# Kernel tuning notes

Measured on AMD Instinct MI355X. Metric: run time of the kernel, lower is better.

## Reference

```python
import jax, jax.numpy as jnp
import numpy as np

N, NFEAT = 8192, 128

def _unif(k, shape, fan_out):
    s = 1.0 / np.sqrt(fan_out)
    return jax.random.uniform(k, shape, jnp.float32, -s, s)

def setup_inputs() -> dict:
    key = jax.random.key(0)
    ks = jax.random.split(key, 10)
    x = jax.random.normal(ks[0], (N, NFEAT), jnp.float32)
    adj = jax.random.uniform(ks[1], (N, N), jnp.float32)  # all > 0 -> full degree
    W1 = _unif(ks[2], (NFEAT, 10), 10); b1 = _unif(ks[3], (10,), 10)
    W2 = _unif(ks[4], (10, 5), 5);      b2 = _unif(ks[5], (5,), 5)
    fc1_W = _unif(ks[6], (5, 5), 5);    fc1_b = _unif(ks[7], (5,), 5)
    fc_W = _unif(ks[8], (5, 2), 2);     fc_b = _unif(ks[9], (2,), 2)
    return dict(x=x, adj=adj, W1=W1, b1=b1, W2=W2, b2=b2,
                fc1_W=fc1_W, fc1_b=fc1_b, fc_W=fc_W, fc_b=fc_b)

def _gcn(x, adj, W, b):
    # D = diag(row-wise count of adj > 0); A_tilda = D^-1/2 (A + I) D^-1/2
    deg = jnp.sum((adj > 0.0).astype(x.dtype), axis=1)
    dinv = deg ** -0.5                       # [N]
    s = (x @ W) * dinv[:, None]              # D^-1/2 @ (X W), [N, out]
    out = dinv[:, None] * (adj @ s + s)      # D^-1/2 @ (A + I) @ s
    return out + b

def reference(x, adj, W1, b1, W2, b2, fc1_W, fc1_b, fc_W, fc_b):
    h = jax.nn.relu(_gcn(x, adj, W1, b1))    # [N, 10]
    h = _gcn(h, adj, W2, b2)                 # [N, 5]
    z = jax.nn.relu(jnp.mean(h, axis=0))     # [5]
    z2 = jax.nn.relu(z @ fc1_W + fc1_b)      # [5]
    y = jax.nn.sigmoid(z2 @ fc_W + fc_b)     # [2]
    return (z, y)
```

## Files before the change

kernel.cpp:

```cpp
#include <hip/hip_runtime.h>
#include <math.h>

#define NN 8192
#define NF 128


__device__ __forceinline__ float comp4(const float4& v, int c) {
    return c == 0 ? v.x : c == 1 ? v.y : c == 2 ? v.z : v.w;
}

__global__ __launch_bounds__(256) void kS1p(const float* __restrict__ x,
                                            const float* __restrict__ W1,
                                            float* __restrict__ s1p) {
    __shared__ float sW[NF * 10];
    for (int i = threadIdx.x; i < NF * 10; i += 256) sW[i] = W1[i];
    __syncthreads();
    int tid = blockIdx.x * 256 + threadIdx.x;
    int j = tid / 10, k = tid % 10;
    const float4* xr = (const float4*)(x + (size_t)j * NF);
    float s = 0.f;
#pragma unroll
    for (int f4 = 0; f4 < 32; f4++) {
        float4 a = xr[f4];
        s += a.x * sW[(f4 * 4 + 0) * 10 + k] + a.y * sW[(f4 * 4 + 1) * 10 + k]
           + a.z * sW[(f4 * 4 + 2) * 10 + k] + a.w * sW[(f4 * 4 + 3) * 10 + k];
    }
    s1p[tid] = s;
}

__global__ __launch_bounds__(512) void kFuse(const float* __restrict__ adj,
                                             const float* __restrict__ s1p,
                                             float* __restrict__ accO,
                                             float* __restrict__ dinv,
                                             float* __restrict__ c0,
                                             int* __restrict__ Zcount,
                                             int* __restrict__ Zlist) {
    __shared__ float lcs[4][2048];
    const int t = threadIdx.x;
    const int lane = t & 63, wid = t >> 6;
    for (int n = t; n < 8192; n += 512) ((float*)lcs)[n] = 0.f;
    __syncthreads();

    const int i0 = blockIdx.x * 32 + wid * 4;
    float acc[4][10];
#pragma unroll
    for (int r = 0; r < 4; r++)
#pragma unroll
        for (int k = 0; k < 10; k++) acc[r][k] = 0.f;
    float rmin[4] = {1e30f, 1e30f, 1e30f, 1e30f};

    const float4* a0p = (const float4*)(adj + (size_t)(i0 + 0) * NN);
    const float4* a1p = (const float4*)(adj + (size_t)(i0 + 1) * NN);
    const float4* a2p = (const float4*)(adj + (size_t)(i0 + 2) * NN);
    const float4* a3p = (const float4*)(adj + (size_t)(i0 + 3) * NN);
    const float4* spB = (const float4*)s1p;

    auto loadT = [&](float4 (&A)[4], float4 (&S)[10], int v) {
        A[0] = a0p[v]; A[1] = a1p[v]; A[2] = a2p[v]; A[3] = a3p[v];
#pragma unroll
        for (int q = 0; q < 10; q++) S[q] = spB[(size_t)v * 10 + q];
    };

    auto computeT = [&](const float4 (&A)[4], const float4 (&S)[10], int v) {
        atomicAdd(&lcs[0][v], A[0].x + A[1].x + A[2].x + A[3].x);
        atomicAdd(&lcs[1][v], A[0].y + A[1].y + A[2].y + A[3].y);
        atomicAdd(&lcs[2][v], A[0].z + A[1].z + A[2].z + A[3].z);
        atomicAdd(&lcs[3][v], A[0].w + A[1].w + A[2].w + A[3].w);
#pragma unroll
        for (int r = 0; r < 4; r++)
            rmin[r] = fminf(rmin[r], fminf(fminf(A[r].x, A[r].y), fminf(A[r].z, A[r].w)));
#pragma unroll
        for (int jj = 0; jj < 4; jj++) {
            const float a0c = comp4(A[0], jj), a1c = comp4(A[1], jj);
            const float a2c = comp4(A[2], jj), a3c = comp4(A[3], jj);
#pragma unroll
            for (int k = 0; k < 10; k++) {
                const int idx = jj * 10 + k;
                const float s = comp4(S[idx >> 2], idx & 3);
                acc[0][k] = fmaf(a0c, s, acc[0][k]);
                acc[1][k] = fmaf(a1c, s, acc[1][k]);
                acc[2][k] = fmaf(a2c, s, acc[2][k]);
                acc[3][k] = fmaf(a3c, s, acc[3][k]);
            }
        }
    };

    float4 Aa[4], Ba[4];
    float4 As[10], Bs[10];
    int vi = lane;
    loadT(Aa, As, vi);
#pragma unroll 1
    for (int it = 0; it < 15; it++) {
        loadT(Ba, Bs, vi + 64);
        computeT(Aa, As, vi);
        loadT(Aa, As, vi + 128);
        computeT(Ba, Bs, vi + 64);
        vi += 128;
    }
    loadT(Ba, Bs, vi + 64);
    computeT(Aa, As, vi);
    computeT(Ba, Bs, vi + 64);

#pragma unroll
    for (int r = 0; r < 4; r++)
#pragma unroll
        for (int k = 0; k < 10; k++)
#pragma unroll
            for (int off = 32; off > 0; off >>= 1)
                acc[r][k] += __shfl_xor(acc[r][k], off, 64);

    const float dinv0 = rsqrtf((float)NN);
#pragma unroll
    for (int r = 0; r < 4; r++) {
        unsigned long long anyz = __ballot(rmin[r] <= 0.f);
        if (lane == 0) {
            const int i = i0 + r;
            dinv[i] = dinv0;
            if (anyz) { int p = atomicAdd(Zcount, 1); Zlist[p] = i; }
#pragma unroll
            for (int k = 0; k < 10; k++) accO[i * 10 + k] = acc[r][k];
        }
    }

    __syncthreads();
    for (int n = t; n < 8192; n += 512)
        atomicAdd(&c0[n], lcs[n & 3][n >> 2]);
}

__global__ __launch_bounds__(256) void kZdeg(const float* __restrict__ adj,
                                             const int* __restrict__ Zcount,
                                             const int* __restrict__ Zlist,
                                             float* __restrict__ dinv) {
    __shared__ int wsum[4];
    const int lane = threadIdx.x & 63, wid = threadIdx.x >> 6;
    const int zc = *Zcount;
    for (int p = blockIdx.x; p < zc; p += gridDim.x) {
        const int zi = Zlist[p];
        const float4* ar = (const float4*)(adj + (size_t)zi * NN);
        int cnt = 0;
        for (int v = threadIdx.x; v < 2048; v += 256) {
            float4 a = ar[v];
            cnt += (a.x > 0.f) + (a.y > 0.f) + (a.z > 0.f) + (a.w > 0.f);
        }
#pragma unroll
        for (int off = 32; off > 0; off >>= 1) cnt += __shfl_xor(cnt, off, 64);
        if (lane == 0) wsum[wid] = cnt;
        __syncthreads();
        if (threadIdx.x == 0)
            dinv[zi] = rsqrtf((float)(wsum[0] + wsum[1] + wsum[2] + wsum[3]));
        __syncthreads();
    }
}

__global__ __launch_bounds__(256) void kTail(const float* __restrict__ adj,
                                             const float* __restrict__ accI,
                                             const float* __restrict__ s1p,
                                             const float* __restrict__ dinv,
                                             const float* __restrict__ c0,
                                             const int* __restrict__ Zcount,
                                             const int* __restrict__ Zlist,
                                             const float* __restrict__ b1,
                                             const float* __restrict__ W2,
                                             float* __restrict__ accum) {
    const int j = blockIdx.x * 256 + threadIdx.x;
    const float dinv0 = rsqrtf((float)NN);
    const float dj = dinv[j];
    float cj = c0[j] * dinv0;
    float hv[10];
#pragma unroll
    for (int k = 0; k < 10; k++) hv[k] = dinv0 * accI[j * 10 + k];

    const int zc = *Zcount;
    for (int p = 0; p < zc; p++) {
        const int zi = Zlist[p];
        const float dz = dinv[zi] - dinv0;
        cj += dz * adj[(size_t)zi * NN + j];
        const float az = dz * adj[(size_t)j * NN + zi];
#pragma unroll
        for (int k = 0; k < 10; k++) hv[k] += az * s1p[zi * 10 + k];
    }
#pragma unroll
    for (int k = 0; k < 10; k++)
        hv[k] = fmaxf(dj * (hv[k] + dj * s1p[j * 10 + k]) + b1[k], 0.f);

    float p10[10];
#pragma unroll
    for (int k = 0; k < 5; k++) {
        float s = 0.f;
#pragma unroll
        for (int m = 0; m < 10; m++) s += hv[m] * W2[m * 5 + k];
        s *= dj;
        p10[k] = cj * s;
        p10[5 + k] = dj * s;
    }
#pragma unroll
    for (int q = 0; q < 10; q++) {
        float v = p10[q];
#pragma unroll
        for (int off = 32; off > 0; off >>= 1) v += __shfl_xor(v, off, 64);
        if ((threadIdx.x & 63) == 0) atomicAdd(&accum[q], v);
    }
}

__global__ void kF2(const float* __restrict__ accum, const float* __restrict__ b2,
                    const float* __restrict__ fc1W, const float* __restrict__ fc1b,
                    const float* __restrict__ fcW, const float* __restrict__ fcb,
                    float* __restrict__ out) {
    if (threadIdx.x == 0 && blockIdx.x == 0) {
        float z[5];
        for (int k = 0; k < 5; k++) {
            float v = (accum[k] + accum[5 + k]) * (1.f / (float)NN) + b2[k];
            z[k] = fmaxf(v, 0.f);
            out[k] = z[k];
        }
        float z2[5];
        for (int m = 0; m < 5; m++) {
            float v = fc1b[m];
            for (int k = 0; k < 5; k++) v += z[k] * fc1W[k * 5 + m];
            z2[m] = fmaxf(v, 0.f);
        }
        for (int n = 0; n < 2; n++) {
            float v = fcb[n];
            for (int m = 0; m < 5; m++) v += z2[m] * fcW[m * 2 + n];
            out[5 + n] = 1.f / (1.f + expf(-v));
        }
    }
}

extern "C" void kernel_launch(void* const* d_in, const int* in_sizes, int n_in,
                              void* d_out, int out_size, void* d_ws, size_t ws_size,
                              hipStream_t stream) {
    const float* x    = (const float*)d_in[0];
    const float* adj  = (const float*)d_in[1];
    const float* W1   = (const float*)d_in[2];
    const float* b1   = (const float*)d_in[3];
    const float* W2   = (const float*)d_in[4];
    const float* b2   = (const float*)d_in[5];
    const float* fc1W = (const float*)d_in[6];
    const float* fc1b = (const float*)d_in[7];
    const float* fcW  = (const float*)d_in[8];
    const float* fcb  = (const float*)d_in[9];
    (void)in_sizes; (void)n_in; (void)out_size; (void)ws_size;

    float* ws    = (float*)d_ws;
    float* dinv  = ws;
    float* c0    = ws + 8192;
    float* accum = ws + 16384;
    int*   Zcount = (int*)(ws + 16394);
    float* s1p   = ws + 16416;
    float* acc   = ws + 98336;
    int*   Zlist  = (int*)(ws + 180256);
    float* out = (float*)d_out;

    hipMemsetAsync(c0, 0, (8192 + 32) * sizeof(float), stream);

    kS1p <<<320, 256, 0, stream>>>(x, W1, s1p);
    kFuse<<<256, 512, 0, stream>>>(adj, s1p, acc, dinv, c0, Zcount, Zlist);
    kZdeg<<<16,  256, 0, stream>>>(adj, Zcount, Zlist, dinv);
    kTail<<<32,  256, 0, stream>>>(adj, acc, s1p, dinv, c0, Zcount, Zlist, b1, W2, accum);
    kF2  <<<1,   64,  0, stream>>>(accum, b2, fc1W, fc1b, fcW, fcb, out);
}
```

Baseline: 446.3 us.

## Fuse degree counting and final MLP into kernels, deepen adjacency load pipeline

Counts non-positive adjacency entries per row inside the main streaming kernel so exact degrees are computed there, removing the separate re-read kernel for zero rows. The final tiny MLP is folded into the tail kernel via a last-block completion counter, removing another launch. The main loop moves from double to triple buffering of adjacency and s1p tiles, with a two-blocks-per-CU launch bound. The extra buffers and occupancy hint raise register pressure and may cause spills.

```diff
diff --git a/kernel.cpp b/kernel.cpp
--- a/kernel.cpp
+++ b/kernel.cpp
@@ -28,13 +28,13 @@
     s1p[tid] = s;
 }
 
-__global__ __launch_bounds__(512) void kFuse(const float* __restrict__ adj,
-                                             const float* __restrict__ s1p,
-                                             float* __restrict__ accO,
-                                             float* __restrict__ dinv,
-                                             float* __restrict__ c0,
-                                             int* __restrict__ Zcount,
-                                             int* __restrict__ Zlist) {
+__global__ __launch_bounds__(512, 2) void kFuse(const float* __restrict__ adj,
+                                                const float* __restrict__ s1p,
+                                                float* __restrict__ accO,
+                                                float* __restrict__ dinv,
+                                                float* __restrict__ c0,
+                                                int* __restrict__ Zcount,
+                                                int* __restrict__ Zlist) {
     __shared__ float lcs[4][2048];
     const int t = threadIdx.x;
     const int lane = t & 63, wid = t >> 6;
@@ -47,7 +47,7 @@
     for (int r = 0; r < 4; r++)
 #pragma unroll
         for (int k = 0; k < 10; k++) acc[r][k] = 0.f;
-    float rmin[4] = {1e30f, 1e30f, 1e30f, 1e30f};
+    int cz[4] = {0, 0, 0, 0};
 
     const float4* a0p = (const float4*)(adj + (size_t)(i0 + 0) * NN);
     const float4* a1p = (const float4*)(adj + (size_t)(i0 + 1) * NN);
@@ -68,7 +68,7 @@
         atomicAdd(&lcs[3][v], A[0].w + A[1].w + A[2].w + A[3].w);
 #pragma unroll
         for (int r = 0; r < 4; r++)
-            rmin[r] = fminf(rmin[r], fminf(fminf(A[r].x, A[r].y), fminf(A[r].z, A[r].w)));
+            cz[r] += (A[r].x <= 0.f) + (A[r].y <= 0.f) + (A[r].z <= 0.f) + (A[r].w <= 0.f);
 #pragma unroll
         for (int jj = 0; jj < 4; jj++) {
             const float a0c = comp4(A[0], jj), a1c = comp4(A[1], jj);
@@ -85,38 +85,39 @@
         }
     };
 
-    float4 Aa[4], Ba[4];
-    float4 As[10], Bs[10];
+    float4 Aa[4], Ab[4], Ac[4];
+    float4 Sa[10], Sb[10], Sc[10];
     int vi = lane;
-    loadT(Aa, As, vi);
+    loadT(Aa, Sa, vi);
+    loadT(Ab, Sb, vi + 64);
 #pragma unroll 1
-    for (int it = 0; it < 15; it++) {
-        loadT(Ba, Bs, vi + 64);
-        computeT(Aa, As, vi);
-        loadT(Aa, As, vi + 128);
-        computeT(Ba, Bs, vi + 64);
-        vi += 128;
-    }
-    loadT(Ba, Bs, vi + 64);
-    computeT(Aa, As, vi);
-    computeT(Ba, Bs, vi + 64);
-
-#pragma unroll
-    for (int r = 0; r < 4; r++)
+    for (int it = 0; it < 10; it++) {
+        loadT(Ac, Sc, vi + 128); computeT(Aa, Sa, vi);
+        loadT(Aa, Sa, vi + 192); computeT(Ab, Sb, vi + 64);
+        loadT(Ab, Sb, vi + 256); computeT(Ac, Sc, vi + 128);
+        vi += 192;
+    }
+    computeT(Aa, Sa, vi);
+    computeT(Ab, Sb, vi + 64);
+
+#pragma unroll
+    for (int r = 0; r < 4; r++) {
 #pragma unroll
         for (int k = 0; k < 10; k++)
 #pragma unroll
             for (int off = 32; off > 0; off >>= 1)
                 acc[r][k] += __shfl_xor(acc[r][k], off, 64);
-
-    const float dinv0 = rsqrtf((float)NN);
-#pragma unroll
-    for (int r = 0; r < 4; r++) {
-        unsigned long long anyz = __ballot(rmin[r] <= 0.f);
-        if (lane == 0) {
+#pragma unroll
+        for (int off = 32; off > 0; off >>= 1)
+            cz[r] += __shfl_xor(cz[r], off, 64);
+    }
+
+    if (lane == 0) {
+#pragma unroll
+        for (int r = 0; r < 4; r++) {
             const int i = i0 + r;
-            dinv[i] = dinv0;
-            if (anyz) { int p = atomicAdd(Zcount, 1); Zlist[p] = i; }
+            dinv[i] = rsqrtf((float)(NN - cz[r]));
+            if (cz[r] != 0) { int p = atomicAdd(Zcount, 1); Zlist[p] = i; }
 #pragma unroll
             for (int k = 0; k < 10; k++) accO[i * 10 + k] = acc[r][k];
         }
@@ -125,31 +126,6 @@
     __syncthreads();
     for (int n = t; n < 8192; n += 512)
         atomicAdd(&c0[n], lcs[n & 3][n >> 2]);
-}
-
-__global__ __launch_bounds__(256) void kZdeg(const float* __restrict__ adj,
-                                             const int* __restrict__ Zcount,
-                                             const int* __restrict__ Zlist,
-                                             float* __restrict__ dinv) {
-    __shared__ int wsum[4];
-    const int lane = threadIdx.x & 63, wid = threadIdx.x >> 6;
-    const int zc = *Zcount;
-    for (int p = blockIdx.x; p < zc; p += gridDim.x) {
-        const int zi = Zlist[p];
-        const float4* ar = (const float4*)(adj + (size_t)zi * NN);
-        int cnt = 0;
-        for (int v = threadIdx.x; v < 2048; v += 256) {
-            float4 a = ar[v];
-            cnt += (a.x > 0.f) + (a.y > 0.f) + (a.z > 0.f) + (a.w > 0.f);
-        }
-#pragma unroll
-        for (int off = 32; off > 0; off >>= 1) cnt += __shfl_xor(cnt, off, 64);
-        if (lane == 0) wsum[wid] = cnt;
-        __syncthreads();
-        if (threadIdx.x == 0)
-            dinv[zi] = rsqrtf((float)(wsum[0] + wsum[1] + wsum[2] + wsum[3]));
-        __syncthreads();
-    }
 }
 
 __global__ __launch_bounds__(256) void kTail(const float* __restrict__ adj,
@@ -161,7 +137,14 @@
                                              const int* __restrict__ Zlist,
                                              const float* __restrict__ b1,
                                              const float* __restrict__ W2,
-                                             float* __restrict__ accum) {
+                                             float* __restrict__ accum,
+                                             int* __restrict__ done,
+                                             const float* __restrict__ b2,
+                                             const float* __restrict__ fc1W,
+                                             const float* __restrict__ fc1b,
+                                             const float* __restrict__ fcW,
+                                             const float* __restrict__ fcb,
+                                             float* __restrict__ out) {
     const int j = blockIdx.x * 256 + threadIdx.x;
     const float dinv0 = rsqrtf((float)NN);
     const float dj = dinv[j];
@@ -200,29 +183,31 @@
         for (int off = 32; off > 0; off >>= 1) v += __shfl_xor(v, off, 64);
         if ((threadIdx.x & 63) == 0) atomicAdd(&accum[q], v);
     }
-}
-
-__global__ void kF2(const float* __restrict__ accum, const float* __restrict__ b2,
-                    const float* __restrict__ fc1W, const float* __restrict__ fc1b,
-                    const float* __restrict__ fcW, const float* __restrict__ fcb,
-                    float* __restrict__ out) {
-    if (threadIdx.x == 0 && blockIdx.x == 0) {
-        float z[5];
-        for (int k = 0; k < 5; k++) {
-            float v = (accum[k] + accum[5 + k]) * (1.f / (float)NN) + b2[k];
-            z[k] = fmaxf(v, 0.f);
-            out[k] = z[k];
-        }
-        float z2[5];
-        for (int m = 0; m < 5; m++) {
-            float v = fc1b[m];
-            for (int k = 0; k < 5; k++) v += z[k] * fc1W[k * 5 + m];
-            z2[m] = fmaxf(v, 0.f);
-        }
-        for (int n = 0; n < 2; n++) {
-            float v = fcb[n];
-            for (int m = 0; m < 5; m++) v += z2[m] * fcW[m * 2 + n];
-            out[5 + n] = 1.f / (1.f + expf(-v));
+
+    __syncthreads();
+    if (threadIdx.x == 0) {
+        __threadfence();
+        if (atomicAdd(done, 1) == 31) {
+            float a10[10];
+#pragma unroll
+            for (int q = 0; q < 10; q++) a10[q] = atomicAdd(&accum[q], 0.f);
+            float z[5];
+            for (int k = 0; k < 5; k++) {
+                float v = (a10[k] + a10[5 + k]) * (1.f / (float)NN) + b2[k];
+                z[k] = fmaxf(v, 0.f);
+                out[k] = z[k];
+            }
+            float z2[5];
+            for (int m = 0; m < 5; m++) {
+                float v = fc1b[m];
+                for (int k = 0; k < 5; k++) v += z[k] * fc1W[k * 5 + m];
+                z2[m] = fmaxf(v, 0.f);
+            }
+            for (int n = 0; n < 2; n++) {
+                float v = fcb[n];
+                for (int m = 0; m < 5; m++) v += z2[m] * fcW[m * 2 + n];
+                out[5 + n] = 1.f / (1.f + expf(-v));
+            }
         }
     }
 }
@@ -247,6 +232,7 @@
     float* c0    = ws + 8192;
     float* accum = ws + 16384;
     int*   Zcount = (int*)(ws + 16394);
+    int*   done   = (int*)(ws + 16395);
     float* s1p   = ws + 16416;
     float* acc   = ws + 98336;
     int*   Zlist  = (int*)(ws + 180256);
@@ -256,7 +242,6 @@
 
     kS1p <<<320, 256, 0, stream>>>(x, W1, s1p);
     kFuse<<<256, 512, 0, stream>>>(adj, s1p, acc, dinv, c0, Zcount, Zlist);
-    kZdeg<<<16,  256, 0, stream>>>(adj, Zcount, Zlist, dinv);
-    kTail<<<32,  256, 0, stream>>>(adj, acc, s1p, dinv, c0, Zcount, Zlist, b1, W2, accum);
-    kF2  <<<1,   64,  0, stream>>>(accum, b2, fc1W, fc1b, fcW, fcb, out);
-}
+    kTail<<<32,  256, 0, stream>>>(adj, acc, s1p, dinv, c0, Zcount, Zlist, b1, W2,
+                                   accum, done, b2, fc1W, fc1b, fcW, fcb, out);
+}
```

Result: slower. 479.7 us (+7.5%).
